# Kernel optimization log

Hardware: AMD Instinct MI355X
Metric: run time of the kernel (lower is better)

Reference implementation:

```python
import jax, jax.numpy as jnp
import numpy as np

B, L, DIM, H = 2, 2048, 2048, 16
DH = DIM // H  # 128, size_per_head


def setup_inputs() -> dict:
    key = jax.random.key(0)
    k1, k2, k3, k4, k5, k6 = jax.random.split(key, 6)
    s = 0.02
    return {
        "query_tensor": jax.random.normal(k1, (B, L, DIM), jnp.float32),
        "value_tensor": jax.random.normal(k2, (B, L, DIM), jnp.float32),
        "attention_mask": jax.random.randint(k3, (B, L), 0, 2).astype(jnp.float32),
        "Wq": jax.random.normal(k4, (DIM, DIM), jnp.float32) * s,
        "Wk": jax.random.normal(k5, (DIM, DIM), jnp.float32) * s,
        "Wv": jax.random.normal(k6, (DIM, DIM), jnp.float32) * s,
    }


def reference(query_tensor, value_tensor, attention_mask, Wq, Wk, Wv):
    b, lq, dim = query_tensor.shape
    lv = value_tensor.shape[1]
    # torch Linear: x @ W.T (no bias)
    q = query_tensor @ Wq.T   # [B, Lq, DIM]
    k = value_tensor @ Wk.T   # [B, Lv, DIM]
    v = value_tensor @ Wv.T   # [B, Lv, DIM]
    # split heads -> [B, H, L, DH]
    q = q.reshape(b, lq, H, DH).transpose(0, 2, 1, 3)
    k = k.reshape(b, lv, H, DH).transpose(0, 2, 1, 3)
    v = v.reshape(b, lv, H, DH).transpose(0, 2, 1, 3)
    scores = jnp.einsum('bhqd,bhkd->bhqk', q, k) / jnp.sqrt(jnp.float32(DH))
    # multiplicative per-query mask, broadcast [B,1,Lq,1] -> [B,H,Lq,Lv]
    scores = scores * attention_mask[:, None, :, None]
    probs = jax.nn.softmax(scores, axis=-1)
    attn = jnp.einsum('bhqk,bhkd->bhqd', probs, v)  # [B,H,Lq,DH]
    return attn.transpose(0, 2, 1, 3).reshape(b, lq, dim)
```

## Files before the change

kernel.cpp:

```cpp
#include <hip/hip_runtime.h>
#include <hip/hip_bf16.h>
#include <stdint.h>

#define DIM_ 2048
#define L_   2048
#define B_   2
#define H_   16
#define DH_  128
#define NT_  32

#define QSCALE_ 0.12751743f

typedef __attribute__((ext_vector_type(4))) float fp32x4;
typedef __attribute__((ext_vector_type(8))) short s16x8;

__device__ __forceinline__ unsigned short bf16_rne(float f) {
    unsigned u = __builtin_bit_cast(unsigned, f);
    u += 0x7fffu + ((u >> 16) & 1u);
    return (unsigned short)(u >> 16);
}

__device__ __forceinline__ fp32x4 MFMA(s16x8 a, s16x8 b, fp32x4 c) {
    return __builtin_amdgcn_mfma_f32_16x16x32_bf16(a, b, c, 0, 0, 0);
}

__device__ __forceinline__ void gld16(const void* g, void* l) {
    auto gp = reinterpret_cast<const uint32_t __attribute__((address_space(1)))*>(
        reinterpret_cast<uintptr_t>(g));
    auto lp = reinterpret_cast<uint32_t __attribute__((address_space(3)))*>(
        reinterpret_cast<uintptr_t>(l));
    __builtin_amdgcn_global_load_lds(gp, lp, 16, 0, 0);
}

__device__ __forceinline__ float exp2_raw(float x) {
    float r; asm("v_exp_f32 %0, %1" : "=v"(r) : "v"(x)); return r;
}

__device__ __forceinline__ unsigned cvtpk_bf16(float a, float b) {
    unsigned r; asm("v_cvt_pk_bf16_f32 %0, %1, %2" : "=v"(r) : "v"(a), "v"(b)); return r;
}

__global__ void __launch_bounds__(256)
cvt_all(const float* __restrict__ query, const float* __restrict__ value,
        const float* __restrict__ Wq, const float* __restrict__ Wk,
        const float* __restrict__ Wv,
        unsigned short* __restrict__ qb, unsigned short* __restrict__ vb,
        unsigned short* __restrict__ wqb, unsigned short* __restrict__ wkb,
        unsigned short* __restrict__ wvb)
{
    const int total4 = 7340032;
    int i = blockIdx.x * 256 + threadIdx.x;
    const int stride = gridDim.x * 256;
    for (; i < total4; i += stride) {
        const float4* s; ushort4* d; int off; float sc = 1.0f;
        if (i < 2097152)      { s = (const float4*)query; d = (ushort4*)qb;  off = i; }
        else if (i < 4194304) { s = (const float4*)value; d = (ushort4*)vb;  off = i - 2097152; }
        else if (i < 5242880) { s = (const float4*)Wq;    d = (ushort4*)wqb; off = i - 4194304; sc = QSCALE_; }
        else if (i < 6291456) { s = (const float4*)Wk;    d = (ushort4*)wkb; off = i - 5242880; }
        else                  { s = (const float4*)Wv;    d = (ushort4*)wvb; off = i - 6291456; }
        float4 v = s[off];
        ushort4 o;
        o.x = bf16_rne(v.x * sc); o.y = bf16_rne(v.y * sc);
        o.z = bf16_rne(v.z * sc); o.w = bf16_rne(v.w * sc);
        d[off] = o;
    }
}

__global__ void __launch_bounds__(512, 2)
gemm_qkv8(const unsigned short* __restrict__ qb, const unsigned short* __restrict__ vb,
          const unsigned short* __restrict__ wqb, const unsigned short* __restrict__ wkb,
          const unsigned short* __restrict__ wvb, const float* __restrict__ mask,
          unsigned short* __restrict__ q_ws, unsigned short* __restrict__ k_ws,
          unsigned short* __restrict__ v_ws)
{
    __shared__ __align__(16) char As_[2][2][16384];
    __shared__ __align__(16) char Bs_[2][2][16384];

    const int tid  = threadIdx.x;
    const int lane = tid & 63;
    const int wid  = tid >> 6;
    const int wm   = wid >> 2;
    const int wn   = wid & 3;
    const int lr   = lane & 15;
    const int lg   = lane >> 4;

    const int g     = (blockIdx.x & 7) * 48 + (blockIdx.x >> 3);
    const int which = g >> 7;
    const int rb    = g & 127;
    const int bm    = (rb >> 3) << 8;
    const int bn    = (rb & 7) << 8;

    const unsigned short* Xb = (which == 0) ? qb : vb;
    const unsigned short* Wb = (which == 0) ? wqb : (which == 1) ? wkb : wvb;

    const int srow = tid >> 2;
    const int sgc  = (tid & 3) ^ (srow & 3);
    const unsigned short* gA = Xb + (size_t)(bm + srow) * DIM_ + sgc * 8;
    const unsigned short* gB = Wb + (size_t)(bn + srow) * DIM_ + sgc * 8;
    const int ldst = wid * 1024;

    const int xsw  = (lg ^ (lr & 3)) << 4;
    const int aoff = (wm * 128 + lr) * 64 + xsw;
    const int boff = (wn * 64 + lr) * 64 + xsw;

    fp32x4 acc[8][4] = {};
    s16x8 bq[4];

#define STG(SLOT, GPTR, T, KK) do {                                              \
    gld16((GPTR) + (size_t)(T) * 64 + (KK) * 32, (SLOT) + ldst);                 \
    gld16((GPTR) + (size_t)128 * DIM_ + (size_t)(T) * 64 + (KK) * 32,            \
          (SLOT) + 8192 + ldst);                                                 \
} while (0)

#define LDA(P, K, MS, MI) (*reinterpret_cast<const s16x8*>(&As_[P][K][aoff + (MS)*4096 + (MI)*1024]))
#define LDB(P, K, NF)     (*reinterpret_cast<const s16x8*>(&Bs_[P][K][boff + (NF)*1024]))

#define PHASE(P, K, MS, LOADB, STAGE_STMT, TAIL_STMT) do {                        \
    s16x8 a0 = LDA(P, K, MS, 0), a1 = LDA(P, K, MS, 1),                          \
          a2 = LDA(P, K, MS, 2), a3 = LDA(P, K, MS, 3);                          \
    if (LOADB) {                                                                  \
        bq[0] = LDB(P, K, 0); bq[1] = LDB(P, K, 1);                              \
        bq[2] = LDB(P, K, 2); bq[3] = LDB(P, K, 3);                              \
    }                                                                             \
    STAGE_STMT;                                                                   \
    __builtin_amdgcn_s_barrier();                                                 \
    asm volatile("s_waitcnt lgkmcnt(0)" ::: "memory");                            \
    __builtin_amdgcn_s_setprio(1);                                                \
    acc[(MS)*4+0][0] = MFMA(a0, bq[0], acc[(MS)*4+0][0]);                         \
    acc[(MS)*4+0][1] = MFMA(a0, bq[1], acc[(MS)*4+0][1]);                         \
    acc[(MS)*4+0][2] = MFMA(a0, bq[2], acc[(MS)*4+0][2]);                         \
    acc[(MS)*4+0][3] = MFMA(a0, bq[3], acc[(MS)*4+0][3]);                         \
    acc[(MS)*4+1][0] = MFMA(a1, bq[0], acc[(MS)*4+1][0]);                         \
    acc[(MS)*4+1][1] = MFMA(a1, bq[1], acc[(MS)*4+1][1]);                         \
    acc[(MS)*4+1][2] = MFMA(a1, bq[2], acc[(MS)*4+1][2]);                         \
    acc[(MS)*4+1][3] = MFMA(a1, bq[3], acc[(MS)*4+1][3]);                         \
    acc[(MS)*4+2][0] = MFMA(a2, bq[0], acc[(MS)*4+2][0]);                         \
    acc[(MS)*4+2][1] = MFMA(a2, bq[1], acc[(MS)*4+2][1]);                         \
    acc[(MS)*4+2][2] = MFMA(a2, bq[2], acc[(MS)*4+2][2]);                         \
    acc[(MS)*4+2][3] = MFMA(a2, bq[3], acc[(MS)*4+2][3]);                         \
    acc[(MS)*4+3][0] = MFMA(a3, bq[0], acc[(MS)*4+3][0]);                         \
    acc[(MS)*4+3][1] = MFMA(a3, bq[1], acc[(MS)*4+3][1]);                         \
    acc[(MS)*4+3][2] = MFMA(a3, bq[2], acc[(MS)*4+3][2]);                         \
    acc[(MS)*4+3][3] = MFMA(a3, bq[3], acc[(MS)*4+3][3]);                         \
    __builtin_amdgcn_s_setprio(0);                                                \
    TAIL_STMT;                                                                    \
    __builtin_amdgcn_s_barrier();                                                 \
} while (0)

#define W6 asm volatile("s_waitcnt vmcnt(6)" ::: "memory")
#define W4 asm volatile("s_waitcnt vmcnt(4)" ::: "memory")
#define W0 asm volatile("s_waitcnt vmcnt(0)" ::: "memory")

#define TILE(PAR, T, S1, S2, S3, S4, W2STMT, W4STMT) do {                         \
    PHASE(PAR, 0, 0, 1, if (S1) STG(&Bs_[(PAR)^1][0][0], gB, (T)+1, 0), (void)0); \
    PHASE(PAR, 0, 1, 0, if (S2) STG(&As_[(PAR)^1][1][0], gA, (T)+1, 1), W2STMT);  \
    PHASE(PAR, 1, 0, 1, if (S3) STG(&Bs_[(PAR)^1][1][0], gB, (T)+1, 1), (void)0); \
    PHASE(PAR, 1, 1, 0, if (S4) STG(&As_[PAR][0][0],     gA, (T)+2, 0), W4STMT);  \
} while (0)

    STG(&As_[0][0][0], gA, 0, 0);
    STG(&Bs_[0][0][0], gB, 0, 0);
    STG(&As_[0][1][0], gA, 0, 1);
    STG(&Bs_[0][1][0], gB, 0, 1);
    W4;
    STG(&As_[1][0][0], gA, 1, 0);
    __builtin_amdgcn_s_barrier();

    for (int t = 0; t < NT_ - 2; t += 2) {
        TILE(0, t,     1, 1, 1, 1, W6, W6);
        TILE(1, t + 1, 1, 1, 1, 1, W6, W6);
    }
    TILE(0, NT_ - 2, 1, 1, 1, 0, W6, W4);
    TILE(1, NT_ - 1, 0, 0, 0, 0, W0, (void)0);

    const int bb = bm >> 11;
    const size_t bh0 = (size_t)(bb * H_) * (L_ * DH_);
    const int h  = (bn >> 7) + (wn >> 1);
    const size_t bh_base = bh0 + (size_t)h * (L_ * DH_);
    const int dbase = (wn & 1) * 64;
    const int rbase = bm + wm * 128;

    if (which == 2) {
        #pragma unroll
        for (int mf = 0; mf < 8; ++mf) {
            int l0 = (rbase + mf * 16 + lg * 4) & (L_ - 1);
            #pragma unroll
            for (int nf = 0; nf < 4; ++nf) {
                int d = dbase + nf * 16 + lr;
                size_t off = bh_base
                    + (size_t)(((l0 >> 5) * 8 + (d >> 4)) * 512
                    + ((d & 15) + (((l0 >> 3) & 3) << 4)) * 8 + (l0 & 7));
                ushort4 pk;
                pk.x = bf16_rne(acc[mf][nf][0]);
                pk.y = bf16_rne(acc[mf][nf][1]);
                pk.z = bf16_rne(acc[mf][nf][2]);
                pk.w = bf16_rne(acc[mf][nf][3]);
                *reinterpret_cast<ushort4*>(&v_ws[off]) = pk;
            }
        }
    } else if (which == 1) {
        #pragma unroll
        for (int mf = 0; mf < 8; ++mf)
            #pragma unroll
            for (int rr = 0; rr < 4; ++rr) {
                int l = (rbase + mf * 16 + lg * 4 + rr) & (L_ - 1);
                #pragma unroll
                for (int nf = 0; nf < 4; ++nf) {
                    int d = dbase + nf * 16 + lr;
                    size_t off = bh_base
                        + (size_t)(((l >> 4) * 4 + (d >> 5)) * 512
                        + ((l & 15) + (((d >> 3) & 3) << 4)) * 8 + (d & 7));
                    k_ws[off] = bf16_rne(acc[mf][nf][rr]);
                }
            }
    } else {
        const float* mrow = mask + bb * L_;
        #pragma unroll
        for (int mf = 0; mf < 8; ++mf)
            #pragma unroll
            for (int rr = 0; rr < 4; ++rr) {
                int l = (rbase + mf * 16 + lg * 4 + rr) & (L_ - 1);
                float mvv = mrow[l];
                #pragma unroll
                for (int nf = 0; nf < 4; ++nf) {
                    int d = dbase + nf * 16 + lr;
                    q_ws[bh_base + (size_t)l * DH_ + d] = bf16_rne(acc[mf][nf][rr] * mvv);
                }
            }
    }
#undef STG
#undef LDA
#undef LDB
#undef PHASE
#undef TILE
#undef W6
#undef W4
#undef W0
}

__global__ void __launch_bounds__(256, 2)
attn_fused3(const unsigned short* __restrict__ qw, const unsigned short* __restrict__ kfr,
            const unsigned short* __restrict__ vfr, float* __restrict__ out)
{
    __shared__ __align__(16) char Ks[2][16384];
    __shared__ __align__(16) char Pl[4][4608];

    const int tid  = threadIdx.x;
    const int lane = tid & 63;
    const int wid  = tid >> 6;
    const int lr   = lane & 15;
    const int lg   = lane >> 4;

    const int p  = (blockIdx.x & 7) * 64 + (blockIdx.x >> 3);
    const int bh = p >> 4;
    const int qt = p & 15;
    const int b  = bh >> 4;
    const int h  = bh & 15;
    const int q0 = qt * 128 + wid * 32;

    const unsigned short* qbase = qw  + (size_t)bh * (L_ * DH_);
    const unsigned short* kbase = kfr + (size_t)bh * (L_ * DH_);
    const unsigned short* vbase = vfr + (size_t)bh * (L_ * DH_);

    s16x8 qf[2][4];
    #pragma unroll
    for (int qs = 0; qs < 2; ++qs)
        #pragma unroll
        for (int kc = 0; kc < 4; ++kc)
            qf[qs][kc] = *reinterpret_cast<const s16x8*>(
                &qbase[(size_t)(q0 + qs * 16 + lr) * DH_ + kc * 32 + lg * 8]);

    s16x8 ones;
    #pragma unroll
    for (int i = 0; i < 8; ++i) ones[i] = (short)0x3F80;

    fp32x4 acc[2][8] = {};
    fp32x4 racc[2] = {};

    char* P = &Pl[wid][0];

    auto STAGE = [&](int buf, int t) {
        const unsigned short* g = kbase + (size_t)t * 8192;
        #pragma unroll
        for (int c = 0; c < 4; ++c)
            gld16(g + c * 2048 + tid * 8, &Ks[buf][c * 4096 + wid * 1024]);
    };

    STAGE(0, 0);
    __syncthreads();

    for (int t = 0; t < L_ / 64; ++t) {
        const int buf = t & 1;
        if (t + 1 < L_ / 64) STAGE(buf ^ 1, t + 1);

        s16x8 vv0[8], vv1[8];
        #pragma unroll
        for (int ds = 0; ds < 8; ++ds)
            vv0[ds] = *reinterpret_cast<const s16x8*>(
                &vbase[(size_t)t * 8192 + (0 * 8 + ds) * 512 + lane * 8]);

        fp32x4 s2[2][4] = {};
        __builtin_amdgcn_s_setprio(1);
        #pragma unroll
        for (int kvs = 0; kvs < 4; ++kvs)
            #pragma unroll
            for (int kc = 0; kc < 4; ++kc) {
                s16x8 kf = *reinterpret_cast<const s16x8*>(
                    Ks[buf] + (kvs * 4 + kc) * 1024 + lane * 16);
                s2[0][kvs] = MFMA(kf, qf[0][kc], s2[0][kvs]);
                s2[1][kvs] = MFMA(kf, qf[1][kc], s2[1][kvs]);
            }
        __builtin_amdgcn_s_setprio(0);

        #pragma unroll
        for (int qs = 0; qs < 2; ++qs)
            #pragma unroll
            for (int kvs = 0; kvs < 4; ++kvs) {
                float e0 = exp2_raw(s2[qs][kvs][0]);
                float e1 = exp2_raw(s2[qs][kvs][1]);
                float e2 = exp2_raw(s2[qs][kvs][2]);
                float e3 = exp2_raw(s2[qs][kvs][3]);
                uint2 pk;
                pk.x = cvtpk_bf16(e0, e1);
                pk.y = cvtpk_bf16(e2, e3);
                *reinterpret_cast<uint2*>(P + qs * 2304 + lr * 144 + kvs * 32 + lg * 8) = pk;
            }

        #pragma unroll
        for (int ds = 0; ds < 8; ++ds)
            vv1[ds] = *reinterpret_cast<const s16x8*>(
                &vbase[(size_t)t * 8192 + (1 * 8 + ds) * 512 + lane * 8]);

        __builtin_amdgcn_s_setprio(1);
        #pragma unroll
        for (int qs = 0; qs < 2; ++qs) {
            s16x8 pa0 = *reinterpret_cast<const s16x8*>(P + qs * 2304 + lr * 144 + 0 * 64 + lg * 16);
            s16x8 pa1 = *reinterpret_cast<const s16x8*>(P + qs * 2304 + lr * 144 + 1 * 64 + lg * 16);
            racc[qs] = MFMA(pa0, ones, racc[qs]);
            racc[qs] = MFMA(pa1, ones, racc[qs]);
            #pragma unroll
            for (int ds = 0; ds < 8; ++ds) {
                acc[qs][ds] = MFMA(pa0, vv0[ds], acc[qs][ds]);
                acc[qs][ds] = MFMA(pa1, vv1[ds], acc[qs][ds]);
            }
        }
        __builtin_amdgcn_s_setprio(0);

        __syncthreads();
    }

    #pragma unroll
    for (int qs = 0; qs < 2; ++qs) {
        float inv[4];
        #pragma unroll
        for (int r = 0; r < 4; ++r) inv[r] = 1.0f / racc[qs][r];
        #pragma unroll
        for (int ds = 0; ds < 8; ++ds)
            #pragma unroll
            for (int r = 0; r < 4; ++r)
                out[((size_t)(b * L_ + q0 + qs * 16 + lg * 4 + r)) * DIM_ + h * DH_ + ds * 16 + lr]
                    = acc[qs][ds][r] * inv[r];
    }
}

extern "C" void kernel_launch(void* const* d_in, const int* in_sizes, int n_in,
                              void* d_out, int out_size, void* d_ws, size_t ws_size,
                              hipStream_t stream) {
    const float* query = (const float*)d_in[0];
    const float* value = (const float*)d_in[1];
    const float* mask  = (const float*)d_in[2];
    const float* Wq    = (const float*)d_in[3];
    const float* Wk    = (const float*)d_in[4];
    const float* Wv    = (const float*)d_in[5];
    float* out = (float*)d_out;

    const size_t elems  = (size_t)B_ * H_ * L_ * DH_;
    const size_t welems = elems / 2;
    unsigned short* q_ws = (unsigned short*)d_ws;
    unsigned short* k_ws = q_ws + elems;
    unsigned short* v_ws = k_ws + elems;

    unsigned short* qbf  = v_ws + elems;
    unsigned short* vbf  = qbf + elems;
    unsigned short* wqbf = vbf + elems;
    unsigned short* wkbf = wqbf + welems;
    unsigned short* wvbf = wkbf + welems;

    dim3 blk(256, 1, 1);

    cvt_all<<<dim3(2048, 1, 1), blk, 0, stream>>>(query, value, Wq, Wk, Wv,
                                                  qbf, vbf, wqbf, wkbf, wvbf);
    gemm_qkv8<<<dim3(384, 1, 1), dim3(512, 1, 1), 0, stream>>>(
        qbf, vbf, wqbf, wkbf, wvbf, mask, q_ws, k_ws, v_ws);

    attn_fused3<<<dim3(512, 1, 1), blk, 0, stream>>>(q_ws, k_ws, v_ws, out);
}
```

Measured before the change: 216.6 us.

## Retile QKV GEMM to 256x128 blocks with triple-buffered LDS pipeline

The projection GEMM moves from 256x256 block tiles (8 waves as 2x4, 128x64 per wave) to 256x128 tiles (4x2 waves, 64x64 per wave), which doubles the grid to 768 blocks. The K loop becomes a three-stage LDS ring buffer that prefetches two tiles ahead, replacing the double-buffered half-tile phase scheme. The goal is better CU load balance and more latency hiding, at the cost of less operand reuse per block and more global traffic for the activation matrix. Accumulator registers per thread are halved, which may allow higher occupancy.

Result: no change. 214.2 us (-1.1%).

```diff
diff --git a/kernel.cpp b/kernel.cpp
--- a/kernel.cpp
+++ b/kernel.cpp
@@ -73,121 +73,123 @@
           unsigned short* __restrict__ q_ws, unsigned short* __restrict__ k_ws,
           unsigned short* __restrict__ v_ws)
 {
-    __shared__ __align__(16) char As_[2][2][16384];
-    __shared__ __align__(16) char Bs_[2][2][16384];
+    __shared__ __align__(16) char As_[3][32768];
+    __shared__ __align__(16) char Bs_[3][16384];
 
     const int tid  = threadIdx.x;
     const int lane = tid & 63;
     const int wid  = tid >> 6;
-    const int wm   = wid >> 2;
-    const int wn   = wid & 3;
+    const int wm   = wid >> 1;
+    const int wn   = wid & 1;
     const int lr   = lane & 15;
     const int lg   = lane >> 4;
 
-    const int g     = (blockIdx.x & 7) * 48 + (blockIdx.x >> 3);
-    const int which = g >> 7;
-    const int rb    = g & 127;
-    const int bm    = (rb >> 3) << 8;
-    const int bn    = (rb & 7) << 8;
+    const int g     = (blockIdx.x & 7) * 96 + (blockIdx.x >> 3);
+    const int which = g >> 8;
+    const int rb    = g & 255;
+    const int bm    = (rb >> 4) << 8;
+    const int bn    = (rb & 15) << 7;
 
     const unsigned short* Xb = (which == 0) ? qb : vb;
     const unsigned short* Wb = (which == 0) ? wqb : (which == 1) ? wkb : wvb;
 
-    const int srow = tid >> 2;
-    const int sgc  = (tid & 3) ^ (srow & 3);
-    const unsigned short* gA = Xb + (size_t)(bm + srow) * DIM_ + sgc * 8;
-    const unsigned short* gB = Wb + (size_t)(bn + srow) * DIM_ + sgc * 8;
+    const int srow = tid >> 3;
+    const int scol = ((tid & 7) ^ (((tid >> 5) & 1) << 1)) * 8;
+    const unsigned short* gA = Xb + (size_t)(bm + srow) * DIM_ + scol;
+    const unsigned short* gB = Wb + (size_t)(bn + srow) * DIM_ + scol;
     const int ldst = wid * 1024;
 
-    const int xsw  = (lg ^ (lr & 3)) << 4;
-    const int aoff = (wm * 128 + lr) * 64 + xsw;
-    const int boff = (wn * 64 + lr) * 64 + xsw;
-
-    fp32x4 acc[8][4] = {};
-    s16x8 bq[4];
-
-#define STG(SLOT, GPTR, T, KK) do {                                              \
-    gld16((GPTR) + (size_t)(T) * 64 + (KK) * 32, (SLOT) + ldst);                 \
-    gld16((GPTR) + (size_t)128 * DIM_ + (size_t)(T) * 64 + (KK) * 32,            \
-          (SLOT) + 8192 + ldst);                                                 \
+    const int xsw  = ((lr >> 2) & 1) << 5;
+    const int abase = wm * 8192 + lr * 128 + ((lg * 16) ^ xsw);
+    const int bbase = wn * 8192 + lr * 128 + ((lg * 16) ^ xsw);
+
+    fp32x4 acc[4][4] = {};
+
+#define STGH1(BUF, T) do {                                                        \
+    gld16(gA + (size_t)(T) * 64,                 &As_[BUF][ldst]);                \
+    gld16(gA + (size_t)64 * DIM_ + (T) * 64,     &As_[BUF][8192 + ldst]);         \
+    gld16(gB + (size_t)(T) * 64,                 &Bs_[BUF][ldst]);                \
 } while (0)
-
-#define LDA(P, K, MS, MI) (*reinterpret_cast<const s16x8*>(&As_[P][K][aoff + (MS)*4096 + (MI)*1024]))
-#define LDB(P, K, NF)     (*reinterpret_cast<const s16x8*>(&Bs_[P][K][boff + (NF)*1024]))
-
-#define PHASE(P, K, MS, LOADB, STAGE_STMT, TAIL_STMT) do {                        \
-    s16x8 a0 = LDA(P, K, MS, 0), a1 = LDA(P, K, MS, 1),                          \
-          a2 = LDA(P, K, MS, 2), a3 = LDA(P, K, MS, 3);                          \
-    if (LOADB) {                                                                  \
-        bq[0] = LDB(P, K, 0); bq[1] = LDB(P, K, 1);                              \
-        bq[2] = LDB(P, K, 2); bq[3] = LDB(P, K, 3);                              \
-    }                                                                             \
-    STAGE_STMT;                                                                   \
+#define STGH2(BUF, T) do {                                                        \
+    gld16(gA + (size_t)128 * DIM_ + (T) * 64,    &As_[BUF][16384 + ldst]);        \
+    gld16(gA + (size_t)192 * DIM_ + (T) * 64,    &As_[BUF][24576 + ldst]);        \
+    gld16(gB + (size_t)64 * DIM_ + (T) * 64,     &Bs_[BUF][8192 + ldst]);         \
+} while (0)
+
+#define PH(AB, BB, KK, STG_STMT, WAIT_STMT) do {                                  \
+    s16x8 fa0 = *reinterpret_cast<const s16x8*>(&(AB)[abase + (KK)*64]);          \
+    s16x8 fa1 = *reinterpret_cast<const s16x8*>(&(AB)[abase + (KK)*64 + 2048]);   \
+    s16x8 fa2 = *reinterpret_cast<const s16x8*>(&(AB)[abase + (KK)*64 + 4096]);   \
+    s16x8 fa3 = *reinterpret_cast<const s16x8*>(&(AB)[abase + (KK)*64 + 6144]);   \
+    s16x8 fb0 = *reinterpret_cast<const s16x8*>(&(BB)[bbase + (KK)*64]);          \
+    s16x8 fb1 = *reinterpret_cast<const s16x8*>(&(BB)[bbase + (KK)*64 + 2048]);   \
+    s16x8 fb2 = *reinterpret_cast<const s16x8*>(&(BB)[bbase + (KK)*64 + 4096]);   \
+    s16x8 fb3 = *reinterpret_cast<const s16x8*>(&(BB)[bbase + (KK)*64 + 6144]);   \
+    STG_STMT;                                                                     \
     __builtin_amdgcn_s_barrier();                                                 \
     asm volatile("s_waitcnt lgkmcnt(0)" ::: "memory");                            \
     __builtin_amdgcn_s_setprio(1);                                                \
-    acc[(MS)*4+0][0] = MFMA(a0, bq[0], acc[(MS)*4+0][0]);                         \
-    acc[(MS)*4+0][1] = MFMA(a0, bq[1], acc[(MS)*4+0][1]);                         \
-    acc[(MS)*4+0][2] = MFMA(a0, bq[2], acc[(MS)*4+0][2]);                         \
-    acc[(MS)*4+0][3] = MFMA(a0, bq[3], acc[(MS)*4+0][3]);                         \
-    acc[(MS)*4+1][0] = MFMA(a1, bq[0], acc[(MS)*4+1][0]);                         \
-    acc[(MS)*4+1][1] = MFMA(a1, bq[1], acc[(MS)*4+1][1]);                         \
-    acc[(MS)*4+1][2] = MFMA(a1, bq[2], acc[(MS)*4+1][2]);                         \
-    acc[(MS)*4+1][3] = MFMA(a1, bq[3], acc[(MS)*4+1][3]);                         \
-    acc[(MS)*4+2][0] = MFMA(a2, bq[0], acc[(MS)*4+2][0]);                         \
-    acc[(MS)*4+2][1] = MFMA(a2, bq[1], acc[(MS)*4+2][1]);                         \
-    acc[(MS)*4+2][2] = MFMA(a2, bq[2], acc[(MS)*4+2][2]);                         \
-    acc[(MS)*4+2][3] = MFMA(a2, bq[3], acc[(MS)*4+2][3]);                         \
-    acc[(MS)*4+3][0] = MFMA(a3, bq[0], acc[(MS)*4+3][0]);                         \
-    acc[(MS)*4+3][1] = MFMA(a3, bq[1], acc[(MS)*4+3][1]);                         \
-    acc[(MS)*4+3][2] = MFMA(a3, bq[2], acc[(MS)*4+3][2]);                         \
-    acc[(MS)*4+3][3] = MFMA(a3, bq[3], acc[(MS)*4+3][3]);                         \
+    acc[0][0] = MFMA(fa0, fb0, acc[0][0]);                                        \
+    acc[0][1] = MFMA(fa0, fb1, acc[0][1]);                                        \
+    acc[0][2] = MFMA(fa0, fb2, acc[0][2]);                                        \
+    acc[0][3] = MFMA(fa0, fb3, acc[0][3]);                                        \
+    acc[1][0] = MFMA(fa1, fb0, acc[1][0]);                                        \
+    acc[1][1] = MFMA(fa1, fb1, acc[1][1]);                                        \
+    acc[1][2] = MFMA(fa1, fb2, acc[1][2]);                                        \
+    acc[1][3] = MFMA(fa1, fb3, acc[1][3]);                                        \
+    acc[2][0] = MFMA(fa2, fb0, acc[2][0]);                                        \
+    acc[2][1] = MFMA(fa2, fb1, acc[2][1]);                                        \
+    acc[2][2] = MFMA(fa2, fb2, acc[2][2]);                                        \
+    acc[2][3] = MFMA(fa2, fb3, acc[2][3]);                                        \
+    acc[3][0] = MFMA(fa3, fb0, acc[3][0]);                                        \
+    acc[3][1] = MFMA(fa3, fb1, acc[3][1]);                                        \
+    acc[3][2] = MFMA(fa3, fb2, acc[3][2]);                                        \
+    acc[3][3] = MFMA(fa3, fb3, acc[3][3]);                                        \
     __builtin_amdgcn_s_setprio(0);                                                \
-    TAIL_STMT;                                                                    \
+    WAIT_STMT;                                                                    \
     __builtin_amdgcn_s_barrier();                                                 \
 } while (0)
 
 #define W6 asm volatile("s_waitcnt vmcnt(6)" ::: "memory")
-#define W4 asm volatile("s_waitcnt vmcnt(4)" ::: "memory")
 #define W0 asm volatile("s_waitcnt vmcnt(0)" ::: "memory")
 
-#define TILE(PAR, T, S1, S2, S3, S4, W2STMT, W4STMT) do {                         \
-    PHASE(PAR, 0, 0, 1, if (S1) STG(&Bs_[(PAR)^1][0][0], gB, (T)+1, 0), (void)0); \
-    PHASE(PAR, 0, 1, 0, if (S2) STG(&As_[(PAR)^1][1][0], gA, (T)+1, 1), W2STMT);  \
-    PHASE(PAR, 1, 0, 1, if (S3) STG(&Bs_[(PAR)^1][1][0], gB, (T)+1, 1), (void)0); \
-    PHASE(PAR, 1, 1, 0, if (S4) STG(&As_[PAR][0][0],     gA, (T)+2, 0), W4STMT);  \
-} while (0)
-
-    STG(&As_[0][0][0], gA, 0, 0);
-    STG(&Bs_[0][0][0], gB, 0, 0);
-    STG(&As_[0][1][0], gA, 0, 1);
-    STG(&Bs_[0][1][0], gB, 0, 1);
-    W4;
-    STG(&As_[1][0][0], gA, 1, 0);
+    STGH1(0, 0); STGH2(0, 0);
+    STGH1(1, 1); STGH2(1, 1);
+    W6;
     __builtin_amdgcn_s_barrier();
 
-    for (int t = 0; t < NT_ - 2; t += 2) {
-        TILE(0, t,     1, 1, 1, 1, W6, W6);
-        TILE(1, t + 1, 1, 1, 1, 1, W6, W6);
-    }
-    TILE(0, NT_ - 2, 1, 1, 1, 0, W6, W4);
-    TILE(1, NT_ - 1, 0, 0, 0, 0, W0, (void)0);
+    for (int t = 0; t < NT_ - 2; ++t) {
+        char* Ab = &As_[t % 3][0];
+        char* Bb = &Bs_[t % 3][0];
+        const int bnx = (t + 2) % 3;
+        PH(Ab, Bb, 0, STGH1(bnx, t + 2), (void)0);
+        PH(Ab, Bb, 1, STGH2(bnx, t + 2), W6);
+    }
+    {
+        char* Ab = &As_[0][0]; char* Bb = &Bs_[0][0];
+        PH(Ab, Bb, 0, (void)0, (void)0);
+        PH(Ab, Bb, 1, (void)0, W0);
+    }
+    {
+        char* Ab = &As_[1][0]; char* Bb = &Bs_[1][0];
+        PH(Ab, Bb, 0, (void)0, (void)0);
+        PH(Ab, Bb, 1, (void)0, (void)0);
+    }
 
     const int bb = bm >> 11;
     const size_t bh0 = (size_t)(bb * H_) * (L_ * DH_);
-    const int h  = (bn >> 7) + (wn >> 1);
-    const size_t bh_base = bh0 + (size_t)h * (L_ * DH_);
-    const int dbase = (wn & 1) * 64;
-    const int rbase = bm + wm * 128;
+    const int rbase = bm + wm * 64;
+    const int cbase = bn + wn * 64;
 
     if (which == 2) {
         #pragma unroll
-        for (int mf = 0; mf < 8; ++mf) {
+        for (int mf = 0; mf < 4; ++mf) {
             int l0 = (rbase + mf * 16 + lg * 4) & (L_ - 1);
             #pragma unroll
             for (int nf = 0; nf < 4; ++nf) {
-                int d = dbase + nf * 16 + lr;
-                size_t off = bh_base
+                int dc = cbase + nf * 16 + lr;
+                int h = dc >> 7, d = dc & 127;
+                size_t off = bh0 + (size_t)h * (L_ * DH_)
                     + (size_t)(((l0 >> 5) * 8 + (d >> 4)) * 512
                     + ((d & 15) + (((l0 >> 3) & 3) << 4)) * 8 + (l0 & 7));
                 ushort4 pk;
@@ -200,14 +202,15 @@
         }
     } else if (which == 1) {
         #pragma unroll
-        for (int mf = 0; mf < 8; ++mf)
+        for (int mf = 0; mf < 4; ++mf)
             #pragma unroll
             for (int rr = 0; rr < 4; ++rr) {
                 int l = (rbase + mf * 16 + lg * 4 + rr) & (L_ - 1);
                 #pragma unroll
                 for (int nf = 0; nf < 4; ++nf) {
-                    int d = dbase + nf * 16 + lr;
-                    size_t off = bh_base
+                    int dc = cbase + nf * 16 + lr;
+                    int h = dc >> 7, d = dc & 127;
+                    size_t off = bh0 + (size_t)h * (L_ * DH_)
                         + (size_t)(((l >> 4) * 4 + (d >> 5)) * 512
                         + ((l & 15) + (((d >> 3) & 3) << 4)) * 8 + (d & 7));
                     k_ws[off] = bf16_rne(acc[mf][nf][rr]);
@@ -216,25 +219,24 @@
     } else {
         const float* mrow = mask + bb * L_;
         #pragma unroll
-        for (int mf = 0; mf < 8; ++mf)
+        for (int mf = 0; mf < 4; ++mf)
             #pragma unroll
             for (int rr = 0; rr < 4; ++rr) {
                 int l = (rbase + mf * 16 + lg * 4 + rr) & (L_ - 1);
                 float mvv = mrow[l];
                 #pragma unroll
                 for (int nf = 0; nf < 4; ++nf) {
-                    int d = dbase + nf * 16 + lr;
-                    q_ws[bh_base + (size_t)l * DH_ + d] = bf16_rne(acc[mf][nf][rr] * mvv);
+                    int dc = cbase + nf * 16 + lr;
+                    int h = dc >> 7, d = dc & 127;
+                    q_ws[bh0 + (size_t)h * (L_ * DH_) + (size_t)l * DH_ + d]
+                        = bf16_rne(acc[mf][nf][rr] * mvv);
                 }
             }
     }
-#undef STG
-#undef LDA
-#undef LDB
-#undef PHASE
-#undef TILE
+#undef STGH1
+#undef STGH2
+#undef PH
 #undef W6
-#undef W4
 #undef W0
 }
 
@@ -390,7 +392,7 @@
 
     cvt_all<<<dim3(2048, 1, 1), blk, 0, stream>>>(query, value, Wq, Wk, Wv,
                                                   qbf, vbf, wqbf, wkbf, wvbf);
-    gemm_qkv8<<<dim3(384, 1, 1), dim3(512, 1, 1), 0, stream>>>(
+    gemm_qkv8<<<dim3(768, 1, 1), dim3(512, 1, 1), 0, stream>>>(
         qbf, vbf, wqbf, wkbf, wvbf, mask, q_ws, k_ws, v_ws);
 
     attn_fused3<<<dim3(512, 1, 1), blk, 0, stream>>>(q_ws, k_ws, v_ws, out);
```
